# Kernel optimization log

Hardware: AMD Instinct MI355X
Metric: run time of the kernel (lower is better)

## Reference

```python
import jax, jax.numpy as jnp
import numpy as np

D = 128          # model_dim
R = 4            # num_relations
H = 64           # hidden width from num_neurons=[64, 64]
N = 50000        # num nodes
E = 800000       # num edges (avg degree 16)
NUM_NODE_TYPES = 3
UPDATE_NODE_TYPES = (0, 1)  # static update_node_type_indices
# update_edge_type_indices = range(R) (all relations), closed over statically


def setup_inputs() -> dict:
    key = jax.random.key(0)
    ks = jax.random.split(key, 12)
    s = 0.05
    return dict(
        node_feature=jax.random.normal(ks[0], (N, D), jnp.float32),
        src=jax.random.randint(ks[1], (E,), 0, N, dtype=jnp.int32),
        dst=jax.random.randint(ks[2], (E,), 0, N, dtype=jnp.int32),
        edge_type=jax.random.randint(ks[3], (E,), 0, R, dtype=jnp.int32),
        node_type=jax.random.randint(ks[4], (N,), 0, NUM_NODE_TYPES, dtype=jnp.int32),
        # per-relation MLP params, stacked over relations
        W1=jax.random.normal(ks[5], (R, D, H), jnp.float32) * s,
        b1=jnp.zeros((R, H), jnp.float32),
        W2=jax.random.normal(ks[6], (R, H, H), jnp.float32) * s,
        b2=jnp.zeros((R, H), jnp.float32),
        W3=jax.random.normal(ks[7], (R, H, D), jnp.float32) * s,
        b3=jnp.zeros((R, D), jnp.float32),
        # node updater: (R+1)*D -> H -> H -> D
        Wu1=jax.random.normal(ks[8], (D * (R + 1), H), jnp.float32) * s,
        bu1=jnp.zeros((H,), jnp.float32),
        Wu2=jax.random.normal(ks[9], (H, H), jnp.float32) * s,
        bu2=jnp.zeros((H,), jnp.float32),
        Wu3=jax.random.normal(ks[10], (H, D), jnp.float32) * s,
        bu3=jnp.zeros((D,), jnp.float32),
    )


def _mlp(x, W1, b1, W2, b2, W3, b3):
    # MLP with ReLU hidden layers, linear output (torch MLP(in, out, [64,64]))
    h = jax.nn.relu(x @ W1 + b1)
    h = jax.nn.relu(h @ W2 + b2)
    return h @ W3 + b3


def reference(node_feature, src, dst, edge_type, node_type,
              W1, b1, W2, b2, W3, b3, Wu1, bu1, Wu2, bu2, Wu3, bu3):
    n = node_feature.shape[0]
    sf = node_feature[src]  # [E, D] gather source features once

    # DGL send_and_recv only writes aggregated features to nodes that receive
    # at least one message; others are zero-filled. Track in-degree > 0.
    indeg = jax.ops.segment_sum(jnp.ones(dst.shape, node_feature.dtype), dst,
                                num_segments=n)
    has_in = (indeg > 0).astype(node_feature.dtype)[:, None]

    blocks = [jax.nn.relu(node_feature) * has_in]  # first D-block of enc input
    for i in range(W1.shape[0]):  # static loop over relations
        msg = jax.nn.relu(_mlp(sf, W1[i], b1[i], W2[i], b2[i], W3[i], b3[i]))
        msg = msg * (edge_type == i)[:, None]  # zero msg for other relations
        blocks.append(jax.ops.segment_sum(msg, dst, num_segments=n))
    enc = jnp.concatenate(blocks, axis=-1)  # [N, (R+1)*D]

    upd = _mlp(enc, Wu1, bu1, Wu2, bu2, Wu3, bu3)  # [N, D]
    upd_mask = jnp.zeros(node_type.shape, bool)
    for t in UPDATE_NODE_TYPES:
        upd_mask = upd_mask | (node_type == t)
    return jnp.where(upd_mask[:, None], upd, node_feature)
```

## Files before the change

kernel.cpp:

```cpp
#include <hip/hip_runtime.h>
#include <hip/hip_bf16.h>

#define D 128
#define H 64
#define R 4
#define NT 64
#define LDC 132
#define CAP 64

typedef __attribute__((ext_vector_type(8))) short bf16x8;
typedef __attribute__((ext_vector_type(4))) float f32x4;

#define PREL 56
#define PFRAG 512
#define UBASE (R * PREL)
#define UPREL 40
#define NFRAG (UBASE + UPREL)

__device__ __forceinline__ float4 relu4(float4 v) {
    return make_float4(fmaxf(v.x, 0.f), fmaxf(v.y, 0.f), fmaxf(v.z, 0.f), fmaxf(v.w, 0.f));
}

__device__ __forceinline__ unsigned short f2bf_rne(float x) {
    unsigned u = __float_as_uint(x);
    return (unsigned short)((u + 0x7fffu + ((u >> 16) & 1u)) >> 16);
}

__device__ __forceinline__ void split1(float x, short& hi, short& lo) {
    unsigned u = __float_as_uint(x);
    unsigned hb = u & 0xffff0000u;
    float res = x - __uint_as_float(hb);
    hi = (short)(u >> 16);
    lo = (short)(__float_as_uint(res) >> 16);
}

__device__ __forceinline__ void split8(const float* x8, bf16x8& hi, bf16x8& lo) {
#pragma unroll
    for (int i = 0; i < 8; ++i) {
        short h, l;
        split1(x8[i], h, l);
        hi[i] = h; lo[i] = l;
    }
}

__device__ __forceinline__ void load_split_A(const float* ap, bf16x8& ah, bf16x8& al) {
    float x8[8];
    *(float4*)&x8[0] = *(const float4*)ap;
    *(float4*)&x8[4] = *(const float4*)(ap + 4);
    split8(x8, ah, al);
}

template<int KSTEPS>
__device__ __forceinline__ void split_strip_A(const float* Ws, int lane, bf16x8* ah, bf16x8* al) {
#pragma unroll
    for (int ks = 0; ks < KSTEPS; ++ks)
        load_split_A(Ws + (lane & 15) * LDC + ks * 32 + ((lane >> 4) << 3), ah[ks], al[ks]);
}

__device__ __forceinline__ void gload_lds16(const void* g, void* l) {
    __builtin_amdgcn_global_load_lds(
        (const __attribute__((address_space(1))) void*)g,
        (__attribute__((address_space(3))) void*)l, 16, 0, 0);
}

__device__ __forceinline__ void stage_chunk(const short* __restrict__ srcH,
                                            short* BbH, int w, int lane) {
#pragma unroll
    for (int f = w; f < 8; f += 4)
        gload_lds16(srcH + ((size_t)f << 9) + (lane << 3), BbH + (f << 9));
}

template<int NCH, int KSTEPS>
__device__ __forceinline__ void compute_chunk(const bf16x8* ah, const bf16x8* al,
                                              const short* BbH,
                                              const short* __restrict__ BloG,
                                              int lane, f32x4* acc) {
#pragma unroll
    for (int ks = 0; ks < KSTEPS; ++ks) {
        bf16x8 bh[NCH], bl[NCH];
#pragma unroll
        for (int n = 0; n < NCH; ++n) {
            int f = n * KSTEPS + ks;
            bh[n] = *(const bf16x8*)(BbH + ((f * 64 + lane) << 3));
            bl[n] = *(const bf16x8*)(BloG + (((size_t)f * 64 + lane) << 3));
        }
#pragma unroll
        for (int n = 0; n < NCH; ++n) {
            acc[n] = __builtin_amdgcn_mfma_f32_16x16x32_bf16(ah[ks], bh[n], acc[n], 0, 0, 0);
            acc[n] = __builtin_amdgcn_mfma_f32_16x16x32_bf16(ah[ks], bl[n], acc[n], 0, 0, 0);
            acc[n] = __builtin_amdgcn_mfma_f32_16x16x32_bf16(al[ks], bh[n], acc[n], 0, 0, 0);
        }
    }
}

template<int NT_TILES, int KSTEPS>
__device__ __forceinline__ void mfma_layer(const float* Als, int ld,
                                           const short* __restrict__ Bhi,
                                           const short* __restrict__ Blo,
                                           int lane, f32x4* acc) {
#pragma unroll
    for (int ks = 0; ks < KSTEPS; ++ks) {
        bf16x8 ah, al;
        load_split_A(Als + (lane & 15) * ld + ks * 32 + ((lane >> 4) << 3), ah, al);
        bf16x8 bh[NT_TILES], bl[NT_TILES];
#pragma unroll
        for (int n = 0; n < NT_TILES; ++n) {
            int f = n * KSTEPS + ks;
            bh[n] = *(const bf16x8*)(Bhi + (((size_t)f * 64 + lane) << 3));
            bl[n] = *(const bf16x8*)(Blo + (((size_t)f * 64 + lane) << 3));
        }
#pragma unroll
        for (int n = 0; n < NT_TILES; ++n) {
            acc[n] = __builtin_amdgcn_mfma_f32_16x16x32_bf16(ah, bh[n], acc[n], 0, 0, 0);
            acc[n] = __builtin_amdgcn_mfma_f32_16x16x32_bf16(ah, bl[n], acc[n], 0, 0, 0);
            acc[n] = __builtin_amdgcn_mfma_f32_16x16x32_bf16(al, bh[n], acc[n], 0, 0, 0);
        }
    }
}

template<int NT_TILES, int KSTEPS>
__device__ __forceinline__ void mfma_layer_regA(const bf16x8* ah, const bf16x8* al,
                                                const short* __restrict__ Bhi,
                                                const short* __restrict__ Blo,
                                                int lane, f32x4* acc) {
#pragma unroll
    for (int ks = 0; ks < KSTEPS; ++ks) {
        bf16x8 bh[NT_TILES], bl[NT_TILES];
#pragma unroll
        for (int n = 0; n < NT_TILES; ++n) {
            int f = n * KSTEPS + ks;
            bh[n] = *(const bf16x8*)(Bhi + (((size_t)f * 64 + lane) << 3));
            bl[n] = *(const bf16x8*)(Blo + (((size_t)f * 64 + lane) << 3));
        }
#pragma unroll
        for (int n = 0; n < NT_TILES; ++n) {
            acc[n] = __builtin_amdgcn_mfma_f32_16x16x32_bf16(ah[ks], bh[n], acc[n], 0, 0, 0);
            acc[n] = __builtin_amdgcn_mfma_f32_16x16x32_bf16(ah[ks], bl[n], acc[n], 0, 0, 0);
            acc[n] = __builtin_amdgcn_mfma_f32_16x16x32_bf16(al[ks], bh[n], acc[n], 0, 0, 0);
        }
    }
}

template<int NT_TILES>
__device__ __forceinline__ void store_C_lds(const f32x4* acc, const float* __restrict__ bias,
                                            float* Ld, int ld, int lane) {
    int r0 = (lane >> 4) << 2;
#pragma unroll
    for (int n = 0; n < NT_TILES; ++n) {
        int col = n * 16 + (lane & 15);
        float bv = bias[col];
#pragma unroll
        for (int q = 0; q < 4; ++q)
            Ld[(r0 + q) * ld + col] = fmaxf(acc[n][q] + bv, 0.f);
    }
}


__global__ __launch_bounds__(256) void k_wprep(
    const float* __restrict__ W1, const float* __restrict__ W2,
    const float* __restrict__ W3, const float* __restrict__ Wu1,
    const float* __restrict__ Wu2, const float* __restrict__ Wu3,
    short* __restrict__ Phi, short* __restrict__ Plo)
{
    int pair = blockIdx.x;
    const float* src; int KS, NTl, fragbase, ncol;
    if (pair < 16) {
        int r = pair >> 2, mat = pair & 3;
        if (mat == 0)      { src = W1  + (size_t)r * (D * H);       KS = 4; NTl = 4; fragbase = r * PREL + 0;  ncol = 64;  }
        else if (mat == 1) { src = W2  + (size_t)r * (H * H);       KS = 2; NTl = 4; fragbase = r * PREL + 16; ncol = 64;  }
        else if (mat == 2) { src = W3  + (size_t)r * (H * D);       KS = 2; NTl = 8; fragbase = r * PREL + 24; ncol = 128; }
        else               { src = Wu1 + (size_t)(r + 1) * D * H;   KS = 4; NTl = 4; fragbase = r * PREL + 40; ncol = 64;  }
    } else {
        int mat = pair - 16;
        if (mat == 0)      { src = Wu1; KS = 4; NTl = 4; fragbase = UBASE + 0;  ncol = 64;  }
        else if (mat == 1) { src = Wu2; KS = 2; NTl = 4; fragbase = UBASE + 16; ncol = 64;  }
        else               { src = Wu3; KS = 2; NTl = 8; fragbase = UBASE + 24; ncol = 128; }
    }
    int nf = NTl * KS;
    for (int u = threadIdx.x; u < nf * 64; u += 256) {
        int f = u >> 6, lane = u & 63;
        int n = f / KS, ks = f - n * KS;
        int col = n * 16 + (lane & 15);
        int k0 = ks * 32 + ((lane >> 4) << 3);
        size_t dstp = (((size_t)(fragbase + f)) * 64 + (size_t)lane) * 8;
#pragma unroll
        for (int i = 0; i < 8; ++i) {
            short h, l;
            split1(src[(size_t)(k0 + i) * ncol + col], h, l);
            Phi[dstp + i] = h;
            Plo[dstp + i] = l;
        }
    }
}


__global__ __launch_bounds__(384, 3) void k_mlp_fill(
    const float* __restrict__ X,
    const float* __restrict__ b1, const float* __restrict__ b2, const float* __restrict__ b3,
    const short* __restrict__ Phi, const short* __restrict__ Plo,
    unsigned short* __restrict__ U, int N, int tiles,
    const int* __restrict__ src, const int* __restrict__ dst,
    const int* __restrict__ etype, int* __restrict__ cnt,
    int* __restrict__ eidx, int E, int epb)
{
    __shared__ float Bsh[NT * LDC];
    __shared__ short BbH[2][8 * PFRAG];

    const int tid = threadIdx.x;
    const int w = tid >> 6;
    const int bid = blockIdx.x;

    if (w >= 4) {
        int ftid = tid - 256;
        int base = bid * epb;
        int end = base + epb; if (end > E) end = E;
        for (int e = base + ftid; e < end; e += 128) {
            int d = dst[e];
            int p = atomicAdd(&cnt[d], 1);
            if (p < CAP) eidx[(size_t)d * CAP + p] = src[e] * 4 + etype[e];
        }
#pragma unroll
        for (int b = 0; b < 7; ++b) __syncthreads();
        return;
    }

    const int lane = tid & 63;
    const int m16 = w * 16;
    const int r = bid / tiles;
    const int n0 = (bid - r * tiles) * NT;

    const short* PH = Phi + (size_t)(r * PREL) * PFRAG;
    const short* PL = Plo + (size_t)(r * PREL) * PFRAG;
    const float* b1r = b1 + r * H;
    const float* b2r = b2 + r * H;
    const float* b3r = b3 + r * D;

    float* Ws = &Bsh[m16 * LDC];

    stage_chunk(PH,             BbH[0], w, lane);
    stage_chunk(PH + 8 * PFRAG, BbH[1], w, lane);

    bf16x8 ahx[4], alx[4];
    {
        int row = n0 + m16 + (lane & 15);
        const float* xp = X + (size_t)row * D + ((lane >> 4) << 3);
        bool ok = (row < N);
#pragma unroll
        for (int ks = 0; ks < 4; ++ks) {
            float x8[8];
            if (ok) {
                *(float4*)&x8[0] = *(const float4*)(xp + ks * 32);
                *(float4*)&x8[4] = *(const float4*)(xp + ks * 32 + 4);
            } else {
#pragma unroll
                for (int i = 0; i < 8; ++i) x8[i] = 0.f;
            }
            split8(x8, ahx[ks], alx[ks]);
        }
    }
    __syncthreads();

    f32x4 acc[8];
#pragma unroll
    for (int n = 0; n < 4; ++n) acc[n] = (f32x4){0.f, 0.f, 0.f, 0.f};
    compute_chunk<2, 4>(ahx, alx, BbH[0], PL, lane, acc + 0);
    __syncthreads();
    stage_chunk(PH + 16 * PFRAG, BbH[0], w, lane);
    compute_chunk<2, 4>(ahx, alx, BbH[1], PL + 8 * PFRAG, lane, acc + 2);
    store_C_lds<4>(acc, b1r, Ws, LDC, lane);
    __syncthreads();
    stage_chunk(PH + 24 * PFRAG, BbH[1], w, lane);

    bf16x8 a2h[2], a2l[2];
    split_strip_A<2>(Ws, lane, a2h, a2l);
#pragma unroll
    for (int n = 0; n < 4; ++n) acc[n] = (f32x4){0.f, 0.f, 0.f, 0.f};
    compute_chunk<4, 2>(a2h, a2l, BbH[0], PL + 16 * PFRAG, lane, acc);
    store_C_lds<4>(acc, b2r, Ws, LDC, lane);
    __syncthreads();
    stage_chunk(PH + 32 * PFRAG, BbH[0], w, lane);

    bf16x8 a3h[2], a3l[2];
    split_strip_A<2>(Ws, lane, a3h, a3l);
#pragma unroll
    for (int n = 0; n < 8; ++n) acc[n] = (f32x4){0.f, 0.f, 0.f, 0.f};
    compute_chunk<4, 2>(a3h, a3l, BbH[1], PL + 24 * PFRAG, lane, acc + 0);
    __syncthreads();
    stage_chunk(PH + 40 * PFRAG, BbH[1], w, lane);
    compute_chunk<4, 2>(a3h, a3l, BbH[0], PL + 32 * PFRAG, lane, acc + 4);
    store_C_lds<8>(acc, b3r, Ws, LDC, lane);
    __syncthreads();
    stage_chunk(PH + 48 * PFRAG, BbH[0], w, lane);

    bf16x8 auh[4], aul[4];
    split_strip_A<4>(Ws, lane, auh, aul);
    f32x4 accu[4];
#pragma unroll
    for (int n = 0; n < 4; ++n) accu[n] = (f32x4){0.f, 0.f, 0.f, 0.f};
    compute_chunk<2, 4>(auh, aul, BbH[1], PL + 40 * PFRAG, lane, accu + 0);
    __syncthreads();
    compute_chunk<2, 4>(auh, aul, BbH[0], PL + 48 * PFRAG, lane, accu + 2);
    {
        int r0 = (lane >> 4) << 2;
#pragma unroll
        for (int n = 0; n < 4; ++n) {
            int col = n * 16 + (lane & 15);
#pragma unroll
            for (int q = 0; q < 4; ++q) {
                int node = n0 + m16 + r0 + q;
                if (node < N)
                    U[((size_t)node * R + r) * H + col] = f2bf_rne(accu[n][q]);
            }
        }
    }
}


__global__ __launch_bounds__(256) void k_gather(
    const unsigned int* __restrict__ U32,
    const int* __restrict__ cnt, const int* __restrict__ eidx,
    float* __restrict__ S, int N)
{
    const int wid = threadIdx.x >> 6, lane = threadIdx.x & 63;
    const int n = blockIdx.x * 4 + wid;
    if (n >= N) return;
    int g = cnt[n]; if (g > CAP) g = CAP;
    const int* ep = eidx + (size_t)n * CAP;
    const int half = lane >> 5;
    const int c2 = lane & 31;
    float ax = 0.f, ay = 0.f;
    {
        int m = g;
        int v = 0;
        if (lane < m) v = ep[lane];
        for (int j0 = 0; j0 < m; j0 += 16) {
            int lim = m - j0; if (lim > 16) lim = 16;
            unsigned t[8];
#pragma unroll
            for (int p = 0; p < 8; ++p) {
                int vi = __shfl(v, j0 + 2 * p + half);
                bool ok = (2 * p + half) < lim;
                t[p] = ok ? U32[(size_t)vi * 32 + c2] : 0u;
            }
#pragma unroll
            for (int p = 0; p < 8; ++p) {
                ax += __uint_as_float(t[p] << 16);
                ay += __uint_as_float(t[p] & 0xffff0000u);
            }
        }
    }
    ax += __shfl_xor(ax, 32);
    ay += __shfl_xor(ay, 32);
    if (half == 0)
        *(float2*)&S[(size_t)n * H + (c2 << 1)] = make_float2(ax, ay);
}


__global__ __launch_bounds__(256, 4) void k_upd(
    const float* __restrict__ X, const float* __restrict__ S,
    const int* __restrict__ cnt, const int* __restrict__ node_type,
    const short* __restrict__ Phi, const short* __restrict__ Plo,
    const float* __restrict__ bu1, const float* __restrict__ bu2, const float* __restrict__ bu3,
    float* __restrict__ out, int N)
{
    __shared__ float Hsh[NT * LDC];

    const int tid = threadIdx.x;
    const int lane = tid & 63;
    const int w = tid >> 6;
    const int m16 = w * 16;
    const int n0 = blockIdx.x * NT;

    const short* PH = Phi + (size_t)UBASE * PFRAG;
    const short* PL = Plo + (size_t)UBASE * PFRAG;

    float* Ws = &Hsh[m16 * LDC];

    bf16x8 ahx[4], alx[4];
    {
        int row = n0 + m16 + (lane & 15);
        bool ok = (row < N) && (cnt[row] > 0);
        const float* xp = X + (size_t)row * D + ((lane >> 4) << 3);
#pragma unroll
        for (int ks = 0; ks < 4; ++ks) {
            float x8[8];
            if (ok) {
                float4 a = *(const float4*)(xp + ks * 32);
                float4 b = *(const float4*)(xp + ks * 32 + 4);
                a = relu4(a); b = relu4(b);
                *(float4*)&x8[0] = a;
                *(float4*)&x8[4] = b;
            } else {
#pragma unroll
                for (int i = 0; i < 8; ++i) x8[i] = 0.f;
            }
            split8(x8, ahx[ks], alx[ks]);
        }
    }

    f32x4 acc[8];
#pragma unroll
    for (int n = 0; n < 4; ++n) acc[n] = (f32x4){0.f, 0.f, 0.f, 0.f};
    mfma_layer_regA<4, 4>(ahx, alx, PH, PL, lane, acc);
    {
        int r0 = (lane >> 4) << 2;
#pragma unroll
        for (int n = 0; n < 4; ++n) {
            int col = n * 16 + (lane & 15);
            float bv = bu1[col];
#pragma unroll
            for (int q = 0; q < 4; ++q) {
                int node = n0 + m16 + r0 + q;
                float sv = (node < N) ? S[(size_t)node * H + col] : 0.f;
                Ws[(r0 + q) * LDC + col] = fmaxf(acc[n][q] + bv + sv, 0.f);
            }
        }
    }

#pragma unroll
    for (int n = 0; n < 4; ++n) acc[n] = (f32x4){0.f, 0.f, 0.f, 0.f};
    mfma_layer<4, 2>(Ws, LDC, PH + (size_t)16 * PFRAG, PL + (size_t)16 * PFRAG, lane, acc);
    store_C_lds<4>(acc, bu2, Ws, LDC, lane);

#pragma unroll
    for (int n = 0; n < 8; ++n) acc[n] = (f32x4){0.f, 0.f, 0.f, 0.f};
    mfma_layer<8, 2>(Ws, LDC, PH + (size_t)24 * PFRAG, PL + (size_t)24 * PFRAG, lane, acc);
    {
        int r0 = (lane >> 4) << 2;
#pragma unroll
        for (int q = 0; q < 4; ++q) {
            int node = n0 + m16 + r0 + q;
            if (node >= N) continue;
            int t = node_type[node];
#pragma unroll
            for (int n = 0; n < 8; ++n) {
                int col = n * 16 + (lane & 15);
                float o = (t <= 1) ? (acc[n][q] + bu3[col])
                                   : X[(size_t)node * D + col];
                out[(size_t)node * D + col] = o;
            }
        }
    }
}

extern "C" void kernel_launch(void* const* d_in, const int* in_sizes, int n_in,
                              void* d_out, int out_size, void* d_ws, size_t ws_size,
                              hipStream_t stream) {
    const float* X     = (const float*)d_in[0];
    const int*   src   = (const int*)d_in[1];
    const int*   dst   = (const int*)d_in[2];
    const int*   etype = (const int*)d_in[3];
    const int*   ntype = (const int*)d_in[4];
    const float* W1    = (const float*)d_in[5];
    const float* b1    = (const float*)d_in[6];
    const float* W2    = (const float*)d_in[7];
    const float* b2    = (const float*)d_in[8];
    const float* W3    = (const float*)d_in[9];
    const float* b3    = (const float*)d_in[10];
    const float* Wu1   = (const float*)d_in[11];
    const float* bu1   = (const float*)d_in[12];
    const float* Wu2   = (const float*)d_in[13];
    const float* bu2   = (const float*)d_in[14];
    const float* Wu3   = (const float*)d_in[15];
    const float* bu3   = (const float*)d_in[16];
    float* out = (float*)d_out;

    const int N = in_sizes[4];
    const int E = in_sizes[1];

    unsigned short* U = (unsigned short*)d_ws;
    float* S    = (float*)(U + (size_t)N * R * H);
    int* cnt    = (int*)(S + (size_t)N * H);
    int* eidx   = cnt + N;
    short* Phi  = (short*)(eidx + (size_t)N * CAP);
    short* Plo  = Phi + (size_t)NFRAG * PFRAG;

    hipMemsetAsync(cnt, 0, (size_t)N * sizeof(int), stream);

    k_wprep<<<19, 256, 0, stream>>>(W1, W2, W3, Wu1, Wu2, Wu3, Phi, Plo);

    int tiles = (N + NT - 1) / NT;
    int mlpB = tiles * R;
    int epb = (E + mlpB - 1) / mlpB;
    k_mlp_fill<<<mlpB, 384, 0, stream>>>(X, b1, b2, b3, Phi, Plo, U, N, tiles,
                                         src, dst, etype, cnt, eidx, E, epb);
    k_gather<<<(N + 3) / 4, 256, 0, stream>>>((const unsigned int*)U, cnt, eidx, S, N);
    k_upd<<<tiles, 256, 0, stream>>>(X, S, cnt, ntype, Phi, Plo, bu1, bu2, bu3, out, N);
}
```

Measured before the change: 159.4 us.

## Bucket edges into coarse destination bins before per-node CSR scatter

```diff
diff --git a/kernel.cpp b/kernel.cpp
--- a/kernel.cpp
+++ b/kernel.cpp
@@ -7,6 +7,7 @@
 #define NT 64
 #define LDC 132
 #define CAP 64
+#define CCAP 4608
 
 typedef __attribute__((ext_vector_type(8))) short bf16x8;
 typedef __attribute__((ext_vector_type(4))) float f32x4;
@@ -200,8 +201,8 @@
     const short* __restrict__ Phi, const short* __restrict__ Plo,
     unsigned short* __restrict__ U, int N, int tiles,
     const int* __restrict__ src, const int* __restrict__ dst,
-    const int* __restrict__ etype, int* __restrict__ cnt,
-    int* __restrict__ eidx, int E, int epb)
+    const int* __restrict__ etype, int* __restrict__ ccnt,
+    int2* __restrict__ coarse, int E, int epb)
 {
     __shared__ float Bsh[NT * LDC];
     __shared__ short BbH[2][8 * PFRAG];
@@ -216,8 +217,9 @@
         int end = base + epb; if (end > E) end = E;
         for (int e = base + ftid; e < end; e += 128) {
             int d = dst[e];
-            int p = atomicAdd(&cnt[d], 1);
-            if (p < CAP) eidx[(size_t)d * CAP + p] = src[e] * 4 + etype[e];
+            int cb = d >> 8;
+            int p = atomicAdd(&ccnt[cb], 1);
+            if (p < CCAP) coarse[(size_t)cb * CCAP + p] = make_int2(d, src[e] * 4 + etype[e]);
         }
 #pragma unroll
         for (int b = 0; b < 7; ++b) __syncthreads();
@@ -312,6 +314,21 @@
                     U[((size_t)node * R + r) * H + col] = f2bf_rne(accu[n][q]);
             }
         }
+    }
+}
+
+
+__global__ __launch_bounds__(256) void k_scatter(
+    const int2* __restrict__ coarse, const int* __restrict__ ccnt,
+    int* __restrict__ cnt, int* __restrict__ eidx)
+{
+    int b = blockIdx.x;
+    int m = ccnt[b]; if (m > CCAP) m = CCAP;
+    const int2* cp = coarse + (size_t)b * CCAP;
+    for (int i = threadIdx.x; i < m; i += 256) {
+        int2 pr = cp[i];
+        int p = atomicAdd(&cnt[pr.x], 1);
+        if (p < CAP) eidx[(size_t)pr.x * CAP + p] = pr.y;
     }
 }
 
@@ -467,15 +484,18 @@
 
     const int N = in_sizes[4];
     const int E = in_sizes[1];
+    const int NB = (N + 255) >> 8;
 
     unsigned short* U = (unsigned short*)d_ws;
     float* S    = (float*)(U + (size_t)N * R * H);
     int* cnt    = (int*)(S + (size_t)N * H);
-    int* eidx   = cnt + N;
-    short* Phi  = (short*)(eidx + (size_t)N * CAP);
+    int* ccnt   = cnt + N;
+    int* eidx   = ccnt + NB;
+    int2* coarse = (int2*)(eidx + (size_t)N * CAP);
+    short* Phi  = (short*)(coarse + (size_t)NB * CCAP);
     short* Plo  = Phi + (size_t)NFRAG * PFRAG;
 
-    hipMemsetAsync(cnt, 0, (size_t)N * sizeof(int), stream);
+    hipMemsetAsync(cnt, 0, (size_t)(N + NB) * sizeof(int), stream);
 
     k_wprep<<<19, 256, 0, stream>>>(W1, W2, W3, Wu1, Wu2, Wu3, Phi, Plo);
 
@@ -483,7 +503,8 @@
     int mlpB = tiles * R;
     int epb = (E + mlpB - 1) / mlpB;
     k_mlp_fill<<<mlpB, 384, 0, stream>>>(X, b1, b2, b3, Phi, Plo, U, N, tiles,
-                                         src, dst, etype, cnt, eidx, E, epb);
+                                         src, dst, etype, ccnt, coarse, E, epb);
+    k_scatter<<<NB, 256, 0, stream>>>(coarse, ccnt, cnt, eidx);
     k_gather<<<(N + 3) / 4, 256, 0, stream>>>((const unsigned int*)U, cnt, eidx, S, N);
     k_upd<<<tiles, 256, 0, stream>>>(X, S, cnt, ntype, Phi, Plo, bu1, bu2, bu3, out, N);
 }
```

New measurement: 540.8 us. +239.4%, slower.
